# Optimization experiments

Measured on AMD Instinct MI355X. Metric: run time of the kernel, lower is better.

## Reference

```python
import jax, jax.numpy as jnp
import numpy as np

FRACTAL_OUTPUT = (5, 5)            # (a, b); requires 5 * num_kernels == a*b
PERC_THRESHOLD = 0.59275
NEXT_SHAPE = (224, 224)
K_END = int(0.4 * FRACTAL_OUTPUT[0] * FRACTAL_OUTPUT[1] + 1)   # 11
KERNEL_SIZES = list(range(3, K_END + 1, 2))                    # [3,5,7,9,11]


def setup_inputs() -> dict:
    key = jax.random.key(0)
    inputs = jax.random.uniform(key, (64, 224, 224, 3), dtype=jnp.float32) * 255.0
    return {"inputs": inputs}


def _extract_patches(x, k):
    # tf.image.extract_patches(sizes=strides=k, SAME) == zero-pad + space-to-depth
    B, H, W, C = x.shape
    rows, cols = -(-H // k), -(-W // k)
    ph, pw = rows * k - H, cols * k - W
    x = jnp.pad(x, ((0, 0), (ph // 2, ph - ph // 2), (pw // 2, pw - pw // 2), (0, 0)))
    x = x.reshape(B, rows, k, cols, k, C).transpose(0, 1, 3, 2, 4, 5)
    return x.reshape(B * rows * cols, k, k, C), rows * cols


def _binarize(patches, k, ch):
    # distance function: 1 iff |channel value - center pixel channel value| <= k
    center = patches[:, k // 2, k // 2, ch][:, None, None]
    return (jnp.abs(patches[..., ch] - center) <= k).astype(jnp.int32)


def _connected_stats(binp, k):
    # 4-connected components via min-label propagation (== tfa connected_components
    # up to relabeling; we only need #components and max label count incl. background)
    N = binp.shape[0]
    idx = jnp.arange(1, k * k + 1, dtype=jnp.int32).reshape(k, k)
    INF = jnp.int32(k * k + 2)
    lbl0 = jnp.where(binp > 0, idx, 0)

    def step(_, lbl):
        v = jnp.where(binp > 0, lbl, INF)
        pad = lambda a, w: jnp.pad(a, ((0, 0),) + w, constant_values=INF)
        up    = pad(v, ((1, 0), (0, 0)))[:, :-1, :]
        down  = pad(v, ((0, 1), (0, 0)))[:, 1:, :]
        left  = pad(v, ((0, 0), (1, 0)))[:, :, :-1]
        right = pad(v, ((0, 0), (0, 1)))[:, :, 1:]
        m = jnp.minimum(jnp.minimum(v, up), jnp.minimum(jnp.minimum(down, left), right))
        return jnp.where(binp > 0, m, 0)

    lbl = jax.lax.fori_loop(0, k * k, step, lbl0)  # k*k iters guarantee convergence
    ncomp = jnp.sum((binp > 0) & (lbl == idx), axis=(1, 2)).astype(jnp.int32)
    lblf = lbl.reshape(N, k * k)
    cnt = jnp.zeros((N, k * k + 1), jnp.int32).at[jnp.arange(N)[:, None], lblf].add(1)
    return ncomp, cnt.max(axis=1)  # (#components, most-common label count incl bg 0)


def _components(inputs, k, ch):
    B = inputs.shape[0]
    patches, P = _extract_patches(inputs, k)
    binp = _binarize(patches, k, ch)                    # (B*P, k, k)
    ones = binp.sum(axis=(1, 2)).reshape(B, P)          # int counts per patch
    # tf.bincount(minlength=1, maxlength=k*k): bins 0..k*k-1, value k*k dropped
    cnt = jnp.zeros((B, k * k + 1), jnp.float32).at[jnp.arange(B)[:, None], ones].add(1.0)
    prob = cnt[:, : k * k] / P                          # (B, k*k)
    n = jnp.arange(1, k * k + 1, dtype=jnp.float32)
    fd = (prob / n).sum(1)
    m = (prob * n).sum(1)
    m2 = ((prob * prob) * n).sum(1)
    lac = (m2 - m * m) / (m * m)
    perc = ((ones.astype(jnp.float32) / (k * k)) >= PERC_THRESHOLD).astype(jnp.int32)
    acp = perc.sum(1) // P                              # tf integer reduce_mean
    ncomp, marea = _connected_stats(binp, k)
    acn = ncomp.reshape(B, P).sum(1) // P
    acma = marea.reshape(B, P).sum(1) // P
    return jnp.stack([acn.astype(jnp.float32), acp.astype(jnp.float32),
                      acma.astype(jnp.float32), lac, fd], axis=1)   # (B, 5)


def _rearrange(c):
    # group metric-major: all acn over kernels, then acp, acma, lac, fd
    return jnp.concatenate([c[:, mm::5] for mm in range(5)], axis=1)


def reference(inputs):
    B = inputs.shape[0]
    chans = []
    for ch in range(3):
        comps = jnp.concatenate([_components(inputs, k, ch) for k in KERNEL_SIZES], axis=1)
        chans.append(_rearrange(comps).reshape(B, FRACTAL_OUTPUT[0], FRACTAL_OUTPUT[1]))
    out = jnp.stack(chans, axis=3)                      # (B, a, b, 3)
    return jax.image.resize(out, (B, NEXT_SHAPE[0], NEXT_SHAPE[1], 3), method='bilinear')
```

## Files before the change

### kernel.cpp

```cpp
#include <hip/hip_runtime.h>

#define HW 224
#define NIMG 64
#define NPIX ((size_t)NIMG * HW * HW)

struct U128 { unsigned long long lo, hi; };
__device__ __forceinline__ U128 u_or  (U128 a, U128 b){ return {a.lo|b.lo, a.hi|b.hi}; }
__device__ __forceinline__ U128 u_and (U128 a, U128 b){ return {a.lo&b.lo, a.hi&b.hi}; }
__device__ __forceinline__ U128 u_andn(U128 a, U128 b){ return {a.lo&~b.lo, a.hi&~b.hi}; }
__device__ __forceinline__ bool u_eq(U128 a, U128 b){ return a.lo==b.lo && a.hi==b.hi; }
__device__ __forceinline__ bool u_nz(U128 a){ return (a.lo | a.hi) != 0ull; }
__device__ __forceinline__ U128 u_shl(U128 a, int n){
    return { a.lo << n, (a.hi << n) | (a.lo >> (64 - n)) };
}
__device__ __forceinline__ U128 u_shr(U128 a, int n){
    return { (a.lo >> n) | (a.hi << (64 - n)), a.hi >> n };
}
__device__ __forceinline__ int u_pop(U128 a){ return __popcll(a.lo) + __popcll(a.hi); }
__device__ __forceinline__ U128 u_low(U128 a){
    if (a.lo) return { a.lo & (0ull - a.lo), 0ull };
    return { 0ull, a.hi & (0ull - a.hi) };
}


template<int K, int S>
__device__ __forceinline__ void stats_body(const float* __restrict__ img,
                                           float* __restrict__ o,
                                           int hist[4][124], int* sums) {
    constexpr int KK   = K * K;
    constexpr int ROWS = (HW + K - 1) / K;
    constexpr int P    = ROWS * ROWS;
    constexpr int PAD  = (ROWS * K - HW) / 2;
    const int wid = threadIdx.x >> 6;

    U128 leftCol{0,0}, rightCol{0,0};
#pragma unroll
    for (int i = 0; i < K; i++) {
        const int cl = i * K, cr = i * K + K - 1;
        if (cl < 64) leftCol.lo  |= 1ull << cl; else leftCol.hi  |= 1ull << (cl - 64);
        if (cr < 64) rightCol.lo |= 1ull << cr; else rightCol.hi |= 1ull << (cr - 64);
    }

    int t_perc = 0, t_ncomp = 0, t_marea = 0;

    for (int p = threadIdx.x; p < P; p += 256) {
        const int pr = p / ROWS, pc = p - pr * ROWS;
        const int y0 = pr * K - PAD, x0 = pc * K - PAD;
        const float cen = img[((size_t)(y0 + K / 2) * HW + (x0 + K / 2)) * S];

        U128 msk{0, 0};
#pragma unroll
        for (int i = 0; i < K; i++) {
            const int y = y0 + i;
            const bool yin = (unsigned)y < (unsigned)HW;
#pragma unroll
            for (int j = 0; j < K; j++) {
                const int x = x0 + j;
                const bool inb = yin && ((unsigned)x < (unsigned)HW);
                const float v = inb ? img[((size_t)y * HW + x) * S] : 0.0f;
                const unsigned long long bit = (fabsf(v - cen) <= (float)K) ? 1ull : 0ull;
                const int c = i * K + j;
                if (c < 64) msk.lo |= bit << c; else msk.hi |= bit << (c - 64);
            }
        }
        const int ones = u_pop(msk);

        int ncomp = 0, maxsz = 0;
        U128 m = msk;
        while (u_nz(m)) {
            U128 s = u_low(m);
            for (;;) {
                U128 g = s;
                g = u_or(g, u_shl(u_andn(s, rightCol), 1));
                g = u_or(g, u_shr(u_andn(s, leftCol), 1));
                g = u_or(g, u_shl(s, K));
                g = u_or(g, u_shr(s, K));
                g = u_and(g, m);
                if (u_eq(g, s)) break;
                s = g;
            }
            ncomp++;
            const int sz = u_pop(s);
            if (sz > maxsz) maxsz = sz;
            m = u_andn(m, s);
        }

        const int bgcnt = KK - ones;
        const int marea = (bgcnt > maxsz) ? bgcnt : maxsz;

        t_ncomp += ncomp;
        t_marea += marea;
        if ((float)ones / (float)KK >= 0.59275f) t_perc++;
        atomicAdd(&hist[wid][ones], 1);
    }

    atomicAdd(&sums[0], t_perc);
    atomicAdd(&sums[1], t_ncomp);
    atomicAdd(&sums[2], t_marea);
    __syncthreads();

    if (threadIdx.x == 0) {
        const float Pf = (float)P;
        float fd = 0.0f, m1 = 0.0f, m2 = 0.0f;
        for (int s = 0; s < KK; s++) {
            const float prob = (float)(hist[0][s] + hist[1][s] + hist[2][s] + hist[3][s]) / Pf;
            const float n = (float)(s + 1);
            fd += prob / n;
            m1 += prob * n;
            m2 += prob * prob * n;
        }
        const float lac = (m2 - m1 * m1) / (m1 * m1);
        o[0]  = (float)(sums[1] / P);
        o[15] = (float)(sums[0] / P);
        o[30] = (float)(sums[2] / P);
        o[45] = lac;
        o[60] = fd;
    }
}

template<int S>
__global__ __launch_bounds__(256) void fractal_stats(const float* __restrict__ in,
                                                     float* __restrict__ interm) {
    const int b    = blockIdx.x / 15;
    const int rem  = blockIdx.x % 15;
    const int ch   = rem / 5;
    const int kidx = rem % 5;

    __shared__ int hist[4][124];
    __shared__ int sums[3];
    for (int i = threadIdx.x; i < 4 * 124; i += 256) ((int*)hist)[i] = 0;
    if (threadIdx.x < 3) sums[threadIdx.x] = 0;
    __syncthreads();

    const float* img = (S == 1) ? in + ((size_t)ch * NIMG + b) * HW * HW
                                : in + (size_t)b * HW * HW * 3 + ch;
    float* o = interm + (size_t)b * 75 + kidx * 3 + ch;

    switch (kidx) {
        case 0: stats_body<3,  S>(img, o, hist, sums); break;
        case 1: stats_body<5,  S>(img, o, hist, sums); break;
        case 2: stats_body<7,  S>(img, o, hist, sums); break;
        case 3: stats_body<9,  S>(img, o, hist, sums); break;
        case 4: stats_body<11, S>(img, o, hist, sums); break;
    }
}

__global__ __launch_bounds__(256) void deinterleave(const float* __restrict__ in,
                                                    float* __restrict__ planes) {
    const size_t pix = (size_t)blockIdx.x * 256 + threadIdx.x;
    if (pix >= NPIX) return;
    const float v0 = in[pix * 3 + 0];
    const float v1 = in[pix * 3 + 1];
    const float v2 = in[pix * 3 + 2];
    planes[pix]            = v0;
    planes[NPIX + pix]     = v1;
    planes[2 * NPIX + pix] = v2;
}

__global__ __launch_bounds__(256) void fractal_resize(const float* __restrict__ interm,
                                                      float* __restrict__ out, int total) {
    const int idx = blockIdx.x * 256 + threadIdx.x;
    if (idx >= total) return;
    const int ch = idx % 3;
    int t = idx / 3;
    const int x = t % HW; t /= HW;
    const int y = t % HW;
    const int b = t / HW;

    const float sc = 5.0f / 224.0f;
    const float uy = ((float)y + 0.5f) * sc - 0.5f;
    const float ux = ((float)x + 0.5f) * sc - 0.5f;

    const float fy = floorf(uy), fx = floorf(ux);
    const float wy = uy - fy,    wx = ux - fx;
    int y0 = (int)fy, x0 = (int)fx;
    int y1 = y0 + 1,  x1 = x0 + 1;
    if (y0 < 0) y0 = 0; if (x0 < 0) x0 = 0;
    if (y1 > 4) y1 = 4; if (x1 > 4) x1 = 4;

    const float* g = interm + (size_t)b * 75 + ch;
    const float v00 = g[(y0 * 5 + x0) * 3];
    const float v01 = g[(y0 * 5 + x1) * 3];
    const float v10 = g[(y1 * 5 + x0) * 3];
    const float v11 = g[(y1 * 5 + x1) * 3];

    out[idx] = (1.0f - wy) * ((1.0f - wx) * v00 + wx * v01)
             +         wy  * ((1.0f - wx) * v10 + wx * v11);
}

extern "C" void kernel_launch(void* const* d_in, const int* in_sizes, int n_in,
                              void* d_out, int out_size, void* d_ws, size_t ws_size,
                              hipStream_t stream) {
    const float* in = (const float*)d_in[0];
    float* out = (float*)d_out;
    float* interm = (float*)d_ws;

    const size_t planes_off = 19456;
    const size_t need = planes_off + 3 * NPIX * sizeof(float);

    if (ws_size >= need) {
        float* planes = (float*)((char*)d_ws + planes_off);
        deinterleave<<<(int)((NPIX + 255) / 256), 256, 0, stream>>>(in, planes);
        fractal_stats<1><<<NIMG * 15, 256, 0, stream>>>(planes, interm);
    } else {
        fractal_stats<3><<<NIMG * 15, 256, 0, stream>>>(in, interm);
    }
    fractal_resize<<<(out_size + 255) / 256, 256, 0, stream>>>(interm, out, out_size);
}
```

Baseline: 185.9 us.

## Stage patch rows in shared memory, use 64-bit masks, vectorize deinterleave

Each block now loads chunks of patch rows into a shared-memory tile with float4 loads, then builds the binary masks from shared memory rather than through scattered global reads. Masks for k<=7 use a single 64-bit word instead of a 128-bit pair. Isolated pixels are counted up front so the flood-fill loop skips them. The deinterleave kernel now handles four pixels per thread with 16-byte loads and stores. The cost is extra __syncthreads per chunk and about 76KB of shared memory per block, which may limit occupancy.

```diff
diff --git a/kernel.cpp b/kernel.cpp
--- a/kernel.cpp
+++ b/kernel.cpp
@@ -4,7 +4,20 @@
 #define NIMG 64
 #define NPIX ((size_t)NIMG * HW * HW)
 
-struct U128 { unsigned long long lo, hi; };
+typedef unsigned long long u64;
+
+struct U128 { u64 lo, hi; };
+
+__device__ __forceinline__ u64  u_or  (u64 a, u64 b){ return a | b; }
+__device__ __forceinline__ u64  u_and (u64 a, u64 b){ return a & b; }
+__device__ __forceinline__ u64  u_andn(u64 a, u64 b){ return a & ~b; }
+__device__ __forceinline__ bool u_eq(u64 a, u64 b){ return a == b; }
+__device__ __forceinline__ bool u_nz(u64 a){ return a != 0ull; }
+__device__ __forceinline__ u64  u_shl(u64 a, int n){ return a << n; }
+__device__ __forceinline__ u64  u_shr(u64 a, int n){ return a >> n; }
+__device__ __forceinline__ int  u_pop(u64 a){ return __popcll(a); }
+__device__ __forceinline__ u64  u_low(u64 a){ return a & (0ull - a); }
+
 __device__ __forceinline__ U128 u_or  (U128 a, U128 b){ return {a.lo|b.lo, a.hi|b.hi}; }
 __device__ __forceinline__ U128 u_and (U128 a, U128 b){ return {a.lo&b.lo, a.hi&b.hi}; }
 __device__ __forceinline__ U128 u_andn(U128 a, U128 b){ return {a.lo&~b.lo, a.hi&~b.hi}; }
@@ -22,76 +35,132 @@
     return { 0ull, a.hi & (0ull - a.hi) };
 }
 
+template<bool B, class T, class F> struct sel       { using type = T; };
+template<class T, class F>         struct sel<false, T, F> { using type = F; };
+
+template<int K> struct Cfg;
+template<> struct Cfg<3>  { static constexpr int CR = 10; };
+template<> struct Cfg<5>  { static constexpr int CR = 17; };
+template<> struct Cfg<7>  { static constexpr int CR = 8;  };
+template<> struct Cfg<9>  { static constexpr int CR = 9;  };
+template<> struct Cfg<11> { static constexpr int CR = 7;  };
+
+#define TILE_FLOATS 19128
 
 template<int K, int S>
 __device__ __forceinline__ void stats_body(const float* __restrict__ img,
                                            float* __restrict__ o,
-                                           int hist[4][124], int* sums) {
+                                           int hist[4][124], int* sums,
+                                           float* tile) {
     constexpr int KK   = K * K;
     constexpr int ROWS = (HW + K - 1) / K;
     constexpr int P    = ROWS * ROWS;
     constexpr int PAD  = (ROWS * K - HW) / 2;
+    constexpr int W    = ROWS * K;
+    constexpr int CR   = Cfg<K>::CR;
+    constexpr int NCH  = (ROWS + CR - 1) / CR;
+    using M = typename sel<(KK <= 64), u64, U128>::type;
     const int wid = threadIdx.x >> 6;
 
-    U128 leftCol{0,0}, rightCol{0,0};
+    u64 lcl = 0, lch = 0, rcl = 0, rch = 0;
 #pragma unroll
     for (int i = 0; i < K; i++) {
         const int cl = i * K, cr = i * K + K - 1;
-        if (cl < 64) leftCol.lo  |= 1ull << cl; else leftCol.hi  |= 1ull << (cl - 64);
-        if (cr < 64) rightCol.lo |= 1ull << cr; else rightCol.hi |= 1ull << (cr - 64);
-    }
+        if (cl < 64) lcl |= 1ull << cl; else lch |= 1ull << (cl - 64);
+        if (cr < 64) rcl |= 1ull << cr; else rch |= 1ull << (cr - 64);
+    }
+    M leftCol, rightCol;
+    if constexpr (KK <= 64) { leftCol = lcl; rightCol = rcl; }
+    else { leftCol = U128{lcl, lch}; rightCol = U128{rcl, rch}; }
 
     int t_perc = 0, t_ncomp = 0, t_marea = 0;
 
-    for (int p = threadIdx.x; p < P; p += 256) {
-        const int pr = p / ROWS, pc = p - pr * ROWS;
-        const int y0 = pr * K - PAD, x0 = pc * K - PAD;
-        const float cen = img[((size_t)(y0 + K / 2) * HW + (x0 + K / 2)) * S];
-
-        U128 msk{0, 0};
-#pragma unroll
-        for (int i = 0; i < K; i++) {
-            const int y = y0 + i;
-            const bool yin = (unsigned)y < (unsigned)HW;
-#pragma unroll
-            for (int j = 0; j < K; j++) {
-                const int x = x0 + j;
-                const bool inb = yin && ((unsigned)x < (unsigned)HW);
-                const float v = inb ? img[((size_t)y * HW + x) * S] : 0.0f;
-                const unsigned long long bit = (fabsf(v - cen) <= (float)K) ? 1ull : 0ull;
-                const int c = i * K + j;
-                if (c < 64) msk.lo |= bit << c; else msk.hi |= bit << (c - 64);
+    for (int c = 0; c < NCH; ++c) {
+        const int pr0       = c * CR;
+        const int rows_this = (CR <= ROWS - pr0) ? CR : (ROWS - pr0);
+        const int nrows     = rows_this * K;
+        const int ybase     = pr0 * K - PAD;
+        const int total     = nrows * W;
+
+        for (int i = threadIdx.x * 4; i < total; i += 1024) {
+            const int r = i / W, w = i - r * W;
+            const int y = ybase + r;
+            bool fast = false;
+            if constexpr (S == 1) {
+                if (w + 4 <= W && i + 4 <= total) {
+                    const int x = w - PAD;
+                    if ((unsigned)y < (unsigned)HW && x >= 0 && x + 4 <= HW) {
+                        float4 v;
+                        __builtin_memcpy(&v, img + (size_t)y * HW + x, 16);
+                        __builtin_memcpy(tile + i, &v, 16);
+                        fast = true;
+                    }
+                }
+            }
+            if (!fast) {
+#pragma unroll
+                for (int e = 0; e < 4; ++e) {
+                    if (i + e >= total) break;
+                    const int rr = (i + e) / W, ww = (i + e) - rr * W;
+                    const int yy = ybase + rr, xx = ww - PAD;
+                    tile[i + e] = ((unsigned)yy < (unsigned)HW && (unsigned)xx < (unsigned)HW)
+                                  ? img[((size_t)yy * HW + xx) * S] : 0.0f;
+                }
             }
         }
-        const int ones = u_pop(msk);
-
-        int ncomp = 0, maxsz = 0;
-        U128 m = msk;
-        while (u_nz(m)) {
-            U128 s = u_low(m);
-            for (;;) {
-                U128 g = s;
-                g = u_or(g, u_shl(u_andn(s, rightCol), 1));
-                g = u_or(g, u_shr(u_andn(s, leftCol), 1));
-                g = u_or(g, u_shl(s, K));
-                g = u_or(g, u_shr(s, K));
-                g = u_and(g, m);
-                if (u_eq(g, s)) break;
-                s = g;
-            }
-            ncomp++;
-            const int sz = u_pop(s);
-            if (sz > maxsz) maxsz = sz;
-            m = u_andn(m, s);
+        __syncthreads();
+
+        const int pcount = rows_this * ROWS;
+        for (int p = threadIdx.x; p < pcount; p += 256) {
+            const int lpr = p / ROWS, pc = p - lpr * ROWS;
+            const int tb  = lpr * K * W + pc * K;
+            const float cen = tile[tb + (K / 2) * W + (K / 2)];
+
+            M msk;
+            if constexpr (KK <= 64) msk = 0ull; else msk = U128{0, 0};
+#pragma unroll
+            for (int i = 0; i < K; i++) {
+#pragma unroll
+                for (int j = 0; j < K; j++) {
+                    const u64 bit = (fabsf(tile[tb + i * W + j] - cen) <= (float)K) ? 1ull : 0ull;
+                    const int cb = i * K + j;
+                    if constexpr (KK <= 64) msk |= bit << cb;
+                    else { if (cb < 64) msk.lo |= bit << cb; else msk.hi |= bit << (cb - 64); }
+                }
+            }
+            const int ones = u_pop(msk);
+
+            M nbm = u_or(u_or(u_shl(u_andn(msk, rightCol), 1),
+                              u_shr(u_andn(msk, leftCol ), 1)),
+                         u_or(u_shl(msk, K), u_shr(msk, K)));
+            M iso = u_andn(msk, nbm);
+            const int niso = u_pop(iso);
+            int ncomp = niso, maxsz = (niso > 0) ? 1 : 0;
+            M m = u_andn(msk, iso);
+            while (u_nz(m)) {
+                M s = u_low(m);
+                for (;;) {
+                    M g = u_or(s, u_or(u_or(u_shl(u_andn(s, rightCol), 1),
+                                            u_shr(u_andn(s, leftCol ), 1)),
+                                       u_or(u_shl(s, K), u_shr(s, K))));
+                    g = u_and(g, m);
+                    if (u_eq(g, s)) break;
+                    s = g;
+                }
+                ncomp++;
+                const int sz = u_pop(s);
+                if (sz > maxsz) maxsz = sz;
+                m = u_andn(m, s);
+            }
+
+            const int bgcnt = KK - ones;
+            const int marea = (bgcnt > maxsz) ? bgcnt : maxsz;
+            t_ncomp += ncomp;
+            t_marea += marea;
+            if ((float)ones / (float)KK >= 0.59275f) t_perc++;
+            atomicAdd(&hist[wid][ones], 1);
         }
-
-        const int bgcnt = KK - ones;
-        const int marea = (bgcnt > maxsz) ? bgcnt : maxsz;
-
-        t_ncomp += ncomp;
-        t_marea += marea;
-        if ((float)ones / (float)KK >= 0.59275f) t_perc++;
-        atomicAdd(&hist[wid][ones], 1);
+        __syncthreads();
     }
 
     atomicAdd(&sums[0], t_perc);
@@ -126,6 +195,7 @@
     const int ch   = rem / 5;
     const int kidx = rem % 5;
 
+    __shared__ __align__(16) float tile[TILE_FLOATS];
     __shared__ int hist[4][124];
     __shared__ int sums[3];
     for (int i = threadIdx.x; i < 4 * 124; i += 256) ((int*)hist)[i] = 0;
@@ -137,24 +207,28 @@
     float* o = interm + (size_t)b * 75 + kidx * 3 + ch;
 
     switch (kidx) {
-        case 0: stats_body<3,  S>(img, o, hist, sums); break;
-        case 1: stats_body<5,  S>(img, o, hist, sums); break;
-        case 2: stats_body<7,  S>(img, o, hist, sums); break;
-        case 3: stats_body<9,  S>(img, o, hist, sums); break;
-        case 4: stats_body<11, S>(img, o, hist, sums); break;
+        case 0: stats_body<3,  S>(img, o, hist, sums, tile); break;
+        case 1: stats_body<5,  S>(img, o, hist, sums, tile); break;
+        case 2: stats_body<7,  S>(img, o, hist, sums, tile); break;
+        case 3: stats_body<9,  S>(img, o, hist, sums, tile); break;
+        case 4: stats_body<11, S>(img, o, hist, sums, tile); break;
     }
 }
 
 __global__ __launch_bounds__(256) void deinterleave(const float* __restrict__ in,
                                                     float* __restrict__ planes) {
-    const size_t pix = (size_t)blockIdx.x * 256 + threadIdx.x;
+    const size_t pix = ((size_t)blockIdx.x * 256 + threadIdx.x) * 4;
     if (pix >= NPIX) return;
-    const float v0 = in[pix * 3 + 0];
-    const float v1 = in[pix * 3 + 1];
-    const float v2 = in[pix * 3 + 2];
-    planes[pix]            = v0;
-    planes[NPIX + pix]     = v1;
-    planes[2 * NPIX + pix] = v2;
+    float4 a, b, c;
+    __builtin_memcpy(&a, in + pix * 3,     16);
+    __builtin_memcpy(&b, in + pix * 3 + 4, 16);
+    __builtin_memcpy(&c, in + pix * 3 + 8, 16);
+    const float4 p0 = make_float4(a.x, a.w, b.z, c.y);
+    const float4 p1 = make_float4(a.y, b.x, b.w, c.z);
+    const float4 p2 = make_float4(a.z, b.y, c.x, c.w);
+    __builtin_memcpy(planes + pix,            &p0, 16);
+    __builtin_memcpy(planes + NPIX + pix,     &p1, 16);
+    __builtin_memcpy(planes + 2 * NPIX + pix, &p2, 16);
 }
 
 __global__ __launch_bounds__(256) void fractal_resize(const float* __restrict__ interm,
@@ -200,7 +274,7 @@
 
     if (ws_size >= need) {
         float* planes = (float*)((char*)d_ws + planes_off);
-        deinterleave<<<(int)((NPIX + 255) / 256), 256, 0, stream>>>(in, planes);
+        deinterleave<<<(int)(NPIX / 4 / 256), 256, 0, stream>>>(in, planes);
         fractal_stats<1><<<NIMG * 15, 256, 0, stream>>>(planes, interm);
     } else {
         fractal_stats<3><<<NIMG * 15, 256, 0, stream>>>(in, interm);
```

Result: slower. 301.3 us (+62.0%).
